# Kernel tuning notes

Hardware: AMD Instinct MI355X
Metric: run time of the kernel (lower is better)

Reference implementation:

```python
import jax, jax.numpy as jnp
import numpy as np

D_MODEL = 1024
NUM_HEADS = 16
HEAD_DIM = D_MODEL // NUM_HEADS


def setup_inputs() -> dict:
    key = jax.random.key(0)
    ks = jax.random.split(key, 9)
    B, S, D = 2, 2048, D_MODEL
    s = 1.0 / np.sqrt(D)
    return {
        "x": jax.random.normal(ks[0], (B, S, D), dtype=jnp.float32),
        "Wq": jax.random.normal(ks[1], (D, D), dtype=jnp.float32) * s,
        "bq": jnp.zeros((D,), dtype=jnp.float32),
        "Wk": jax.random.normal(ks[2], (D, D), dtype=jnp.float32) * s,
        "bk": jnp.zeros((D,), dtype=jnp.float32),
        "Wv": jax.random.normal(ks[3], (D, D), dtype=jnp.float32) * s,
        "bv": jnp.zeros((D,), dtype=jnp.float32),
        "Wo": jax.random.normal(ks[4], (D, D), dtype=jnp.float32) * s,
        "bo": jnp.zeros((D,), dtype=jnp.float32),
    }


def reference(x, Wq, bq, Wk, bk, Wv, bv, Wo, bo):
    B, S, D = x.shape
    H, Hd = NUM_HEADS, HEAD_DIM
    # Linear projections (torch Linear: x @ W^T + b)
    q = (x @ Wq.T + bq).reshape(B, S, H, Hd).transpose(0, 2, 1, 3)  # [B,H,S,Hd]
    k = (x @ Wk.T + bk).reshape(B, S, H, Hd).transpose(0, 2, 1, 3)
    v = (x @ Wv.T + bv).reshape(B, S, H, Hd).transpose(0, 2, 1, 3)
    scale = 1.0 / jnp.sqrt(jnp.asarray(Hd, dtype=x.dtype))
    scores = jnp.einsum("bhqd,bhkd->bhqk", q, k) * scale  # [B,H,S,S]
    causal = jnp.triu(jnp.ones((S, S), dtype=bool), k=1)  # True above diagonal
    scores = jnp.where(causal[None, None], -jnp.inf, scores)
    attn = jax.nn.softmax(scores, axis=-1)
    out = jnp.einsum("bhqk,bhkd->bhqd", attn, v)  # [B,H,S,Hd]
    out = out.transpose(0, 2, 1, 3).reshape(B, S, D)
    return out @ Wo.T + bo
```

## Files before the change

kernel.cpp:

```cpp
#include <hip/hip_runtime.h>

typedef _Float16 f16x8 __attribute__((ext_vector_type(8)));
typedef _Float16 f16x4 __attribute__((ext_vector_type(4)));
typedef float f32x4 __attribute__((ext_vector_type(4)));

#define MFMA32(a, b, c) __builtin_amdgcn_mfma_f32_16x16x32_f16(a, b, c, 0, 0, 0)
#define MFMA16(a, b, c) __builtin_amdgcn_mfma_f32_16x16x16f16(a, b, c, 0, 0, 0)

__global__ __launch_bounds__(256) void convert_all(
    const float* __restrict__ x,
    const float* __restrict__ w0, const float* __restrict__ w1,
    const float* __restrict__ w2, const float* __restrict__ w3,
    _Float16* __restrict__ xb,
    _Float16* __restrict__ o0, _Float16* __restrict__ o1,
    _Float16* __restrict__ o2, _Float16* __restrict__ o3) {
  int chunk = blockIdx.x * 256 + threadIdx.x;
  const float* in;
  _Float16* out;
  int i;
  if (chunk < 1048576) {
    in = x; out = xb; i = chunk * 4;
  } else {
    int t = chunk - 1048576;
    int z = t >> 18;
    i = (t & 262143) * 4;
    in = (z == 0) ? w0 : (z == 1) ? w1 : (z == 2) ? w2 : w3;
    out = (z == 0) ? o0 : (z == 1) ? o1 : (z == 2) ? o2 : o3;
  }
  float4 v = *(const float4*)(in + i);
  f16x4 h;
  h.x = (_Float16)v.x; h.y = (_Float16)v.y; h.z = (_Float16)v.z; h.w = (_Float16)v.w;
  *(f16x4*)(out + i) = h;
}

__device__ __forceinline__ void gld_lds16(_Float16* l, const _Float16* g) {
  __builtin_amdgcn_global_load_lds(
      (const __attribute__((address_space(1))) unsigned int*)g,
      (__attribute__((address_space(3))) unsigned int*)l, 16, 0, 0);
}

__device__ __forceinline__ void stage64(_Float16* lds, const _Float16* g,
                                        int wid, int lane) {
#pragma unroll
  for (int j = 0; j < 2; ++j) {
    int blk = wid * 2 + j;
    int row = blk * 8 + (lane >> 3);
    int col = (lane & 7) * 8;
    gld_lds16(lds + blk * 512, g + (size_t)row * 1024 + col);
  }
}

__device__ __forceinline__ void stage128(_Float16* lds, const _Float16* g,
                                         int wid, int lane) {
#pragma unroll
  for (int j = 0; j < 4; ++j) {
    int blk = wid * 4 + j;
    int row = blk * 8 + (lane >> 3);
    int col = (lane & 7) * 8;
    gld_lds16(lds + blk * 512, g + (size_t)row * 1024 + col);
  }
}

__device__ __forceinline__ void gemm_core64(const _Float16* __restrict__ A,
                                            const _Float16* __restrict__ W,
                                            _Float16* As, _Float16* Bs,
                                            f32x4 acc[4][2], int m0, int n0, int tid) {
  int lane = tid & 63, wid = tid >> 6;
  int lr = lane & 15, lg = lane >> 4;
  int wn = wid * 32;
  for (int k0 = 0; k0 < 1024; k0 += 64) {
    __syncthreads();
    stage64(As, A + (size_t)m0 * 1024 + k0, wid, lane);
    stage128(Bs, W + (size_t)n0 * 1024 + k0, wid, lane);
    __syncthreads();
#pragma unroll
    for (int ks = 0; ks < 2; ++ks) {
      f16x8 af[4], bfv[2];
#pragma unroll
      for (int mf = 0; mf < 4; ++mf)
        af[mf] = *(const f16x8*)(As + (mf * 16 + lr) * 64 + ks * 32 + lg * 8);
#pragma unroll
      for (int nf = 0; nf < 2; ++nf)
        bfv[nf] = *(const f16x8*)(Bs + (wn + nf * 16 + lr) * 64 + ks * 32 + lg * 8);
#pragma unroll
      for (int mf = 0; mf < 4; ++mf)
#pragma unroll
        for (int nf = 0; nf < 2; ++nf)
          acc[mf][nf] = MFMA32(af[mf], bfv[nf], acc[mf][nf]);
    }
  }
}

#define TRP 72

__global__ __launch_bounds__(256) void proj_gemm(
    const _Float16* __restrict__ xb,
    const _Float16* __restrict__ wq, const _Float16* __restrict__ wk,
    const _Float16* __restrict__ wv,
    const float* __restrict__ bq, const float* __restrict__ bk,
    const float* __restrict__ bv,
    _Float16* __restrict__ qo, _Float16* __restrict__ ko, _Float16* __restrict__ vo) {
  __shared__ __align__(16) _Float16 smem[12288];
  _Float16* As = smem;
  _Float16* Bs = smem + 4096;
  int z = blockIdx.z;
  const _Float16* W = (z == 0) ? wq : ((z == 1) ? wk : wv);
  const float* bias = (z == 0) ? bq : ((z == 1) ? bk : bv);
  int tid = threadIdx.x;
  int m0 = blockIdx.x * 64, n0 = blockIdx.y * 128;
  f32x4 acc[4][2] = {};
  gemm_core64(xb, W, As, Bs, acc, m0, n0, tid);

  int lane = tid & 63, wid = tid >> 6;
  int lr = lane & 15, lg = lane >> 4;
  int wn = wid * 32;

  if (z == 2) {
    _Float16* Tr = smem;
    int b = m0 >> 11, s0 = m0 & 2047;
    __syncthreads();
#pragma unroll
    for (int nf = 0; nf < 2; ++nf) {
      int c = wn + nf * 16 + lr;
      float bb = bias[n0 + c];
#pragma unroll
      for (int mf = 0; mf < 4; ++mf)
#pragma unroll
        for (int i = 0; i < 4; ++i)
          Tr[c * TRP + mf * 16 + lg * 4 + i] = (_Float16)(acc[mf][nf][i] + bb);
    }
    __syncthreads();
#pragma unroll
    for (int j = 0; j < 4; ++j) {
      int cid = tid + 256 * j;
      int c = cid >> 3, seg = cid & 7;
      int cg = n0 + c, h = cg >> 6, hd = cg & 63;
      f16x8 v = *(const f16x8*)(Tr + c * TRP + seg * 8);
      *(f16x8*)(vo + ((size_t)(b * 16 + h) * 64 + hd) * 2048 + s0 + seg * 8) = v;
    }
  } else {
    _Float16* o = (z == 0) ? qo : ko;
#pragma unroll
    for (int nf = 0; nf < 2; ++nf) {
      int col = n0 + wn + nf * 16 + lr;
      float bb = bias[col];
      int h = col >> 6, hd = col & 63;
#pragma unroll
      for (int mf = 0; mf < 4; ++mf)
#pragma unroll
        for (int i = 0; i < 4; ++i) {
          int row = m0 + mf * 16 + lg * 4 + i;
          int b = row >> 11, s = row & 2047;
          o[((size_t)(b * 16 + h) * 2048 + s) * 64 + hd] = (_Float16)(acc[mf][nf][i] + bb);
        }
    }
  }
}

__global__ __launch_bounds__(256) void out_gemm(
    const _Float16* __restrict__ attn, const _Float16* __restrict__ wo,
    const float* __restrict__ bo, float* __restrict__ out) {
  __shared__ __align__(16) _Float16 smem[12288];
  _Float16* As = smem;
  _Float16* Bs = smem + 4096;
  int tid = threadIdx.x;
  int m0 = blockIdx.x * 64, n0 = blockIdx.y * 128;
  f32x4 acc[4][2] = {};
  gemm_core64(attn, wo, As, Bs, acc, m0, n0, tid);

  int lane = tid & 63, wid = tid >> 6;
  int lr = lane & 15, lg = lane >> 4;
  int wn = wid * 32;
#pragma unroll
  for (int nf = 0; nf < 2; ++nf) {
    int col = n0 + wn + nf * 16 + lr;
    float bb = bo[col];
#pragma unroll
    for (int mf = 0; mf < 4; ++mf)
#pragma unroll
      for (int i = 0; i < 4; ++i) {
        int row = m0 + mf * 16 + lg * 4 + i;
        out[(size_t)row * 1024 + col] = acc[mf][nf][i] + bb;
      }
  }
}

#define LDP 72

template <bool MASK>
__device__ __forceinline__ void attn_tile32(const _Float16* Ks, const _Float16* Vs,
                                            const f16x8 qb[2][2], int kv0, int qwb,
                                            int lr, int lg,
                                            float m[2], float l[2], f32x4 ot[2][4]) {
  const float L2E = 1.44269504f;
  const float NINF = -__builtin_inff();
  f16x8 kf0[4], kf1[4];
#pragma unroll
  for (int nf = 0; nf < 4; ++nf) {
    kf0[nf] = *(const f16x8*)(Ks + (nf * 16 + lr) * LDP + lg * 8);
    kf1[nf] = *(const f16x8*)(Ks + (nf * 16 + lr) * LDP + 32 + lg * 8);
  }
  f32x4 sc[2][4];
#pragma unroll
  for (int h = 0; h < 2; ++h)
#pragma unroll
    for (int nf = 0; nf < 4; ++nf) {
      f32x4 z = {0.f, 0.f, 0.f, 0.f};
      z = MFMA32(kf0[nf], qb[h][0], z);
      z = MFMA32(kf1[nf], qb[h][1], z);
      sc[h][nf] = z;
    }
  if (MASK) {
#pragma unroll
    for (int h = 0; h < 2; ++h) {
      int qg = qwb + h * 16 + lr;
#pragma unroll
      for (int nf = 0; nf < 4; ++nf)
#pragma unroll
        for (int i = 0; i < 4; ++i) {
          int kg = kv0 + nf * 16 + lg * 4 + i;
          sc[h][nf][i] = (kg <= qg) ? sc[h][nf][i] : NINF;
        }
    }
  }
  f16x4 pf[2][4];
#pragma unroll
  for (int h = 0; h < 2; ++h) {
    f32x4 mx4 = sc[h][0];
#pragma unroll
    for (int nf = 1; nf < 4; ++nf)
#pragma unroll
      for (int i = 0; i < 4; ++i) mx4[i] = fmaxf(mx4[i], sc[h][nf][i]);
    float tm = fmaxf(fmaxf(mx4[0], mx4[1]), fmaxf(mx4[2], mx4[3]));
    tm = fmaxf(tm, __shfl_xor(tm, 16));
    tm = fmaxf(tm, __shfl_xor(tm, 32));
    float mn = fmaxf(m[h], tm);
    float alpha = __builtin_amdgcn_exp2f((m[h] - mn) * L2E);
    m[h] = mn;
    float mnL = mn * L2E;
    float ps = 0.f;
#pragma unroll
    for (int nf = 0; nf < 4; ++nf)
#pragma unroll
      for (int i = 0; i < 4; ++i) {
        float p = __builtin_amdgcn_exp2f(sc[h][nf][i] * L2E - mnL);
        ps += p;
        pf[h][nf][i] = (_Float16)p;
      }
    ps += __shfl_xor(ps, 16);
    ps += __shfl_xor(ps, 32);
    l[h] = l[h] * alpha + ps;
#pragma unroll
    for (int dt = 0; dt < 4; ++dt)
#pragma unroll
      for (int i = 0; i < 4; ++i) ot[h][dt][i] *= alpha;
  }
#pragma unroll
  for (int nf = 0; nf < 4; ++nf)
#pragma unroll
    for (int dt = 0; dt < 4; ++dt) {
      f16x4 vf = *(const f16x4*)(Vs + (dt * 16 + lr) * LDP + nf * 16 + lg * 4);
      ot[0][dt] = MFMA16(vf, pf[0][nf], ot[0][dt]);
      ot[1][dt] = MFMA16(vf, pf[1][nf], ot[1][dt]);
    }
}

__global__ __launch_bounds__(256) void attn_kernel(
    const _Float16* __restrict__ Q, const _Float16* __restrict__ K,
    const _Float16* __restrict__ VT, _Float16* __restrict__ O) {
  __shared__ __align__(16) _Float16 Ks[2][64 * LDP];
  __shared__ __align__(16) _Float16 Vs[2][64 * LDP];
  int tid = threadIdx.x, lane = tid & 63, wid = tid >> 6;
  int hh = blockIdx.x;
  int qt = blockIdx.z ? (15 - (int)blockIdx.y) : (int)blockIdx.y;
  int b = blockIdx.z;
  size_t hoff = (size_t)(b * 16 + hh) * 2048 * 64;
  const _Float16* Qh = Q + hoff;
  const _Float16* Kh = K + hoff;
  const _Float16* VTh = VT + hoff;
  int qwb = qt * 128 + wid * 32;
  int lr = lane & 15, lg = lane >> 4;

  f16x8 qb[2][2];
#pragma unroll
  for (int h = 0; h < 2; ++h) {
    const _Float16* qp = Qh + (size_t)(qwb + h * 16 + lr) * 64;
    qb[h][0] = *(const f16x8*)(qp + lg * 8);
    qb[h][1] = *(const f16x8*)(qp + 32 + lg * 8);
#pragma unroll
    for (int j = 0; j < 8; ++j) {
      qb[h][0][j] *= (_Float16)0.125f;
      qb[h][1][j] *= (_Float16)0.125f;
    }
  }

  float m[2] = {-__builtin_inff(), -__builtin_inff()};
  float l[2] = {0.f, 0.f};
  f32x4 ot[2][4] = {};

  int r0 = tid >> 3, c0 = (tid & 7) * 8;
  int r1 = r0 + 32;
  int4 rk0 = *(const int4*)(Kh + (size_t)r0 * 64 + c0);
  int4 rk1 = *(const int4*)(Kh + (size_t)r1 * 64 + c0);
  int4 rv0 = *(const int4*)(VTh + (size_t)r0 * 2048 + c0);
  int4 rv1 = *(const int4*)(VTh + (size_t)r1 * 2048 + c0);
  *(int4*)(&Ks[0][0] + r0 * LDP + c0) = rk0;
  *(int4*)(&Ks[0][0] + r1 * LDP + c0) = rk1;
  *(int4*)(&Vs[0][0] + r0 * LDP + c0) = rv0;
  *(int4*)(&Vs[0][0] + r1 * LDP + c0) = rv1;
  __syncthreads();

  int aw = qwb >> 6;
  int ntiles = 2 * qt + 2;
  for (int t = 0; t < ntiles; ++t) {
    int cur = t & 1;
    if (t + 1 < ntiles) {
      int nkv = (t + 1) * 64;
      rk0 = *(const int4*)(Kh + (size_t)(nkv + r0) * 64 + c0);
      rk1 = *(const int4*)(Kh + (size_t)(nkv + r1) * 64 + c0);
      rv0 = *(const int4*)(VTh + (size_t)r0 * 2048 + nkv + c0);
      rv1 = *(const int4*)(VTh + (size_t)r1 * 2048 + nkv + c0);
    }
    if (t < aw)
      attn_tile32<false>(&Ks[cur][0], &Vs[cur][0], qb, t * 64, qwb, lr, lg, m, l, ot);
    else if (t == aw)
      attn_tile32<true>(&Ks[cur][0], &Vs[cur][0], qb, t * 64, qwb, lr, lg, m, l, ot);
    if (t + 1 < ntiles) {
      *(int4*)(&Ks[cur ^ 1][0] + r0 * LDP + c0) = rk0;
      *(int4*)(&Ks[cur ^ 1][0] + r1 * LDP + c0) = rk1;
      *(int4*)(&Vs[cur ^ 1][0] + r0 * LDP + c0) = rv0;
      *(int4*)(&Vs[cur ^ 1][0] + r1 * LDP + c0) = rv1;
    }
    __syncthreads();
  }

#pragma unroll
  for (int h = 0; h < 2; ++h) {
    float inv = 1.f / l[h];
    _Float16* Oh = O + ((size_t)b * 2048 + qwb + h * 16 + lr) * 1024 + hh * 64;
#pragma unroll
    for (int dt = 0; dt < 4; ++dt) {
      f16x4 o;
#pragma unroll
      for (int i = 0; i < 4; ++i) o[i] = (_Float16)(ot[h][dt][i] * inv);
      *(f16x4*)(Oh + dt * 16 + lg * 4) = o;
    }
  }
}

extern "C" void kernel_launch(void* const* d_in, const int* in_sizes, int n_in,
                              void* d_out, int out_size, void* d_ws, size_t ws_size,
                              hipStream_t stream) {
  const float* x  = (const float*)d_in[0];
  const float* Wq = (const float*)d_in[1];
  const float* bq = (const float*)d_in[2];
  const float* Wk = (const float*)d_in[3];
  const float* bk = (const float*)d_in[4];
  const float* Wv = (const float*)d_in[5];
  const float* bv = (const float*)d_in[6];
  const float* Wo = (const float*)d_in[7];
  const float* bo = (const float*)d_in[8];
  float* out = (float*)d_out;

  _Float16* ws  = (_Float16*)d_ws;
  _Float16* xb  = ws;
  _Float16* wqb = ws + 4194304;
  _Float16* wkb = ws + 5242880;
  _Float16* wvb = ws + 6291456;
  _Float16* wob = ws + 7340032;
  _Float16* qw  = ws + 8388608;
  _Float16* kw  = ws + 12582912;
  _Float16* vtw = ws + 16777216;
  _Float16* aw  = ws + 20971520;

  convert_all<<<8192, 256, 0, stream>>>(x, Wq, Wk, Wv, Wo,
                                        xb, wqb, wkb, wvb, wob);

  proj_gemm<<<dim3(64, 8, 3), 256, 0, stream>>>(xb, wqb, wkb, wvb, bq, bk, bv,
                                                qw, kw, vtw);
  attn_kernel<<<dim3(16, 16, 2), 256, 0, stream>>>(qw, kw, vtw, aw);
  out_gemm<<<dim3(64, 8), 256, 0, stream>>>(aw, wob, bo, out);
}
```

Baseline: 123.0 us.

## Fuse Q and K projections into one block sharing the staged x tile

The projection kernel now runs Q and K in the same block. The x tile is staged once into shared memory and feeds two accumulator sets, while V keeps its own path. This removes the duplicate x loads for Q and K and cuts the grid from three z-slices to two. In exchange, shared memory per block grows from 24KB to 40KB and accumulator registers double, which may lower occupancy, and the grid shrinks to 1024 blocks with uneven work per block.

```diff
diff --git a/kernel.cpp b/kernel.cpp
--- a/kernel.cpp
+++ b/kernel.cpp
@@ -100,29 +100,72 @@
     const float* __restrict__ bq, const float* __restrict__ bk,
     const float* __restrict__ bv,
     _Float16* __restrict__ qo, _Float16* __restrict__ ko, _Float16* __restrict__ vo) {
-  __shared__ __align__(16) _Float16 smem[12288];
-  _Float16* As = smem;
-  _Float16* Bs = smem + 4096;
-  int z = blockIdx.z;
-  const _Float16* W = (z == 0) ? wq : ((z == 1) ? wk : wv);
-  const float* bias = (z == 0) ? bq : ((z == 1) ? bk : bv);
+  __shared__ __align__(16) _Float16 smem[20480];
   int tid = threadIdx.x;
-  int m0 = blockIdx.x * 64, n0 = blockIdx.y * 128;
-  f32x4 acc[4][2] = {};
-  gemm_core64(xb, W, As, Bs, acc, m0, n0, tid);
-
   int lane = tid & 63, wid = tid >> 6;
   int lr = lane & 15, lg = lane >> 4;
   int wn = wid * 32;
-
-  if (z == 2) {
+  int m0 = blockIdx.x * 64, n0 = blockIdx.y * 128;
+
+  if (blockIdx.z == 0) {
+    _Float16* As = smem;
+    _Float16* Bq = smem + 4096;
+    _Float16* Bk = smem + 12288;
+    f32x4 aq[4][2] = {}, ak[4][2] = {};
+    for (int k0 = 0; k0 < 1024; k0 += 64) {
+      __syncthreads();
+      stage64(As, xb + (size_t)m0 * 1024 + k0, wid, lane);
+      stage128(Bq, wq + (size_t)n0 * 1024 + k0, wid, lane);
+      stage128(Bk, wk + (size_t)n0 * 1024 + k0, wid, lane);
+      __syncthreads();
+#pragma unroll
+      for (int ks = 0; ks < 2; ++ks) {
+        f16x8 af[4], bqf[2], bkf[2];
+#pragma unroll
+        for (int mf = 0; mf < 4; ++mf)
+          af[mf] = *(const f16x8*)(As + (mf * 16 + lr) * 64 + ks * 32 + lg * 8);
+#pragma unroll
+        for (int nf = 0; nf < 2; ++nf) {
+          bqf[nf] = *(const f16x8*)(Bq + (wn + nf * 16 + lr) * 64 + ks * 32 + lg * 8);
+          bkf[nf] = *(const f16x8*)(Bk + (wn + nf * 16 + lr) * 64 + ks * 32 + lg * 8);
+        }
+#pragma unroll
+        for (int mf = 0; mf < 4; ++mf)
+#pragma unroll
+          for (int nf = 0; nf < 2; ++nf) {
+            aq[mf][nf] = MFMA32(af[mf], bqf[nf], aq[mf][nf]);
+            ak[mf][nf] = MFMA32(af[mf], bkf[nf], ak[mf][nf]);
+          }
+      }
+    }
+#pragma unroll
+    for (int nf = 0; nf < 2; ++nf) {
+      int col = n0 + wn + nf * 16 + lr;
+      float bbq = bq[col], bbk = bk[col];
+      int h = col >> 6, hd = col & 63;
+#pragma unroll
+      for (int mf = 0; mf < 4; ++mf)
+#pragma unroll
+        for (int i = 0; i < 4; ++i) {
+          int row = m0 + mf * 16 + lg * 4 + i;
+          int b = row >> 11, s = row & 2047;
+          size_t off = ((size_t)(b * 16 + h) * 2048 + s) * 64 + hd;
+          qo[off] = (_Float16)(aq[mf][nf][i] + bbq);
+          ko[off] = (_Float16)(ak[mf][nf][i] + bbk);
+        }
+    }
+  } else {
+    _Float16* As = smem;
+    _Float16* Bs = smem + 4096;
+    f32x4 acc[4][2] = {};
+    gemm_core64(xb, wv, As, Bs, acc, m0, n0, tid);
     _Float16* Tr = smem;
     int b = m0 >> 11, s0 = m0 & 2047;
     __syncthreads();
 #pragma unroll
     for (int nf = 0; nf < 2; ++nf) {
       int c = wn + nf * 16 + lr;
-      float bb = bias[n0 + c];
+      float bb = bv[n0 + c];
 #pragma unroll
       for (int mf = 0; mf < 4; ++mf)
 #pragma unroll
@@ -137,22 +180,6 @@
       int cg = n0 + c, h = cg >> 6, hd = cg & 63;
       f16x8 v = *(const f16x8*)(Tr + c * TRP + seg * 8);
       *(f16x8*)(vo + ((size_t)(b * 16 + h) * 64 + hd) * 2048 + s0 + seg * 8) = v;
-    }
-  } else {
-    _Float16* o = (z == 0) ? qo : ko;
-#pragma unroll
-    for (int nf = 0; nf < 2; ++nf) {
-      int col = n0 + wn + nf * 16 + lr;
-      float bb = bias[col];
-      int h = col >> 6, hd = col & 63;
-#pragma unroll
-      for (int mf = 0; mf < 4; ++mf)
-#pragma unroll
-        for (int i = 0; i < 4; ++i) {
-          int row = m0 + mf * 16 + lg * 4 + i;
-          int b = row >> 11, s = row & 2047;
-          o[((size_t)(b * 16 + h) * 2048 + s) * 64 + hd] = (_Float16)(acc[mf][nf][i] + bb);
-        }
     }
   }
 }
@@ -376,7 +403,7 @@
   convert_all<<<8192, 256, 0, stream>>>(x, Wq, Wk, Wv, Wo,
                                         xb, wqb, wkb, wvb, wob);
 
-  proj_gemm<<<dim3(64, 8, 3), 256, 0, stream>>>(xb, wqb, wkb, wvb, bq, bk, bv,
+  proj_gemm<<<dim3(64, 8, 2), 256, 0, stream>>>(xb, wqb, wkb, wvb, bq, bk, bv,
                                                 qw, kw, vtw);
   attn_kernel<<<dim3(16, 16, 2), 256, 0, stream>>>(qw, kw, vtw, aw);
   out_gemm<<<dim3(64, 8), 256, 0, stream>>>(aw, wob, bo, out);
```

New measurement: 126.1 us. +2.6%, slower.

## Split KV tiles across two wave groups per attention block and merge softmax

Applied to the files above, without the earlier changes.

The attention block grows to 512 threads in two groups of four waves. Each group processes alternate 64-key tiles of the same 128 queries, staged in four shared-memory buffers loaded per 128-key step. At the end, group B writes its running max, sum and partial outputs to shared memory, and group A merges them with rescaling before writing the output. This doubles the waves in flight to improve latency hiding and MFMA throughput. It costs an extra combine pass through shared memory and more load imbalance on the causal diagonal.

```diff
diff --git a/kernel.cpp b/kernel.cpp
--- a/kernel.cpp
+++ b/kernel.cpp
@@ -265,12 +265,19 @@
     }
 }
 
-__global__ __launch_bounds__(256) void attn_kernel(
+__global__ __launch_bounds__(512, 4) void attn_kernel(
     const _Float16* __restrict__ Q, const _Float16* __restrict__ K,
     const _Float16* __restrict__ VT, _Float16* __restrict__ O) {
-  __shared__ __align__(16) _Float16 Ks[2][64 * LDP];
-  __shared__ __align__(16) _Float16 Vs[2][64 * LDP];
+  __shared__ __align__(16) _Float16 smem[18432];
+  _Float16* KsA = smem;
+  _Float16* KsB = smem + 4608;
+  _Float16* VsA = smem + 9216;
+  _Float16* VsB = smem + 13824;
+  const float L2E = 1.44269504f;
+
   int tid = threadIdx.x, lane = tid & 63, wid = tid >> 6;
+  int grp = wid >> 2;
+  int wq4 = wid & 3;
   int hh = blockIdx.x;
   int qt = blockIdx.z ? (15 - (int)blockIdx.y) : (int)blockIdx.y;
   int b = blockIdx.z;
@@ -278,7 +285,7 @@
   const _Float16* Qh = Q + hoff;
   const _Float16* Kh = K + hoff;
   const _Float16* VTh = VT + hoff;
-  int qwb = qt * 128 + wid * 32;
+  int qwb = qt * 128 + wq4 * 32;
   int lr = lane & 15, lg = lane >> 4;
 
   f16x8 qb[2][2];
@@ -298,52 +305,79 @@
   float l[2] = {0.f, 0.f};
   f32x4 ot[2][4] = {};
 
-  int r0 = tid >> 3, c0 = (tid & 7) * 8;
-  int r1 = r0 + 32;
-  int4 rk0 = *(const int4*)(Kh + (size_t)r0 * 64 + c0);
-  int4 rk1 = *(const int4*)(Kh + (size_t)r1 * 64 + c0);
-  int4 rv0 = *(const int4*)(VTh + (size_t)r0 * 2048 + c0);
-  int4 rv1 = *(const int4*)(VTh + (size_t)r1 * 2048 + c0);
-  *(int4*)(&Ks[0][0] + r0 * LDP + c0) = rk0;
-  *(int4*)(&Ks[0][0] + r1 * LDP + c0) = rk1;
-  *(int4*)(&Vs[0][0] + r0 * LDP + c0) = rv0;
-  *(int4*)(&Vs[0][0] + r1 * LDP + c0) = rv1;
+  int rr = tid >> 3, cc = (tid & 7) * 8;
+  int4 rka = *(const int4*)(Kh + (size_t)rr * 64 + cc);
+  int4 rkb = *(const int4*)(Kh + (size_t)(64 + rr) * 64 + cc);
+  int4 rva = *(const int4*)(VTh + (size_t)rr * 2048 + cc);
+  int4 rvb = *(const int4*)(VTh + (size_t)rr * 2048 + 64 + cc);
+  *(int4*)(KsA + rr * LDP + cc) = rka;
+  *(int4*)(KsB + rr * LDP + cc) = rkb;
+  *(int4*)(VsA + rr * LDP + cc) = rva;
+  *(int4*)(VsB + rr * LDP + cc) = rvb;
   __syncthreads();
 
   int aw = qwb >> 6;
-  int ntiles = 2 * qt + 2;
-  for (int t = 0; t < ntiles; ++t) {
-    int cur = t & 1;
-    if (t + 1 < ntiles) {
-      int nkv = (t + 1) * 64;
-      rk0 = *(const int4*)(Kh + (size_t)(nkv + r0) * 64 + c0);
-      rk1 = *(const int4*)(Kh + (size_t)(nkv + r1) * 64 + c0);
-      rv0 = *(const int4*)(VTh + (size_t)r0 * 2048 + nkv + c0);
-      rv1 = *(const int4*)(VTh + (size_t)r1 * 2048 + nkv + c0);
-    }
-    if (t < aw)
-      attn_tile32<false>(&Ks[cur][0], &Vs[cur][0], qb, t * 64, qwb, lr, lg, m, l, ot);
-    else if (t == aw)
-      attn_tile32<true>(&Ks[cur][0], &Vs[cur][0], qb, t * 64, qwb, lr, lg, m, l, ot);
-    if (t + 1 < ntiles) {
-      *(int4*)(&Ks[cur ^ 1][0] + r0 * LDP + c0) = rk0;
-      *(int4*)(&Ks[cur ^ 1][0] + r1 * LDP + c0) = rk1;
-      *(int4*)(&Vs[cur ^ 1][0] + r0 * LDP + c0) = rv0;
-      *(int4*)(&Vs[cur ^ 1][0] + r1 * LDP + c0) = rv1;
-    }
+  for (int p = 0; p <= qt; ++p) {
+    if (p < qt) {
+      int ka = (p + 1) * 128, kb = ka + 64;
+      rka = *(const int4*)(Kh + (size_t)(ka + rr) * 64 + cc);
+      rkb = *(const int4*)(Kh + (size_t)(kb + rr) * 64 + cc);
+      rva = *(const int4*)(VTh + (size_t)rr * 2048 + ka + cc);
+      rvb = *(const int4*)(VTh + (size_t)rr * 2048 + kb + cc);
+    }
+    int tm = 2 * p + grp;
+    const _Float16* Ks = grp ? KsB : KsA;
+    const _Float16* Vs = grp ? VsB : VsA;
+    if (tm < aw)
+      attn_tile32<false>(Ks, Vs, qb, tm * 64, qwb, lr, lg, m, l, ot);
+    else if (tm == aw)
+      attn_tile32<true>(Ks, Vs, qb, tm * 64, qwb, lr, lg, m, l, ot);
     __syncthreads();
-  }
-
-#pragma unroll
-  for (int h = 0; h < 2; ++h) {
-    float inv = 1.f / l[h];
-    _Float16* Oh = O + ((size_t)b * 2048 + qwb + h * 16 + lr) * 1024 + hh * 64;
-#pragma unroll
-    for (int dt = 0; dt < 4; ++dt) {
-      f16x4 o;
-#pragma unroll
-      for (int i = 0; i < 4; ++i) o[i] = (_Float16)(ot[h][dt][i] * inv);
-      *(f16x4*)(Oh + dt * 16 + lg * 4) = o;
+    if (p < qt) {
+      *(int4*)(KsA + rr * LDP + cc) = rka;
+      *(int4*)(KsB + rr * LDP + cc) = rkb;
+      *(int4*)(VsA + rr * LDP + cc) = rva;
+      *(int4*)(VsB + rr * LDP + cc) = rvb;
+      __syncthreads();
+    }
+  }
+
+  float* Cmb = (float*)smem;
+  if (grp == 1) {
+    int base = wq4 * 64 + lane;
+#pragma unroll
+    for (int h = 0; h < 2; ++h) {
+      Cmb[(h * 18 + 0) * 256 + base] = m[h];
+      Cmb[(h * 18 + 1) * 256 + base] = l[h];
+#pragma unroll
+      for (int dt = 0; dt < 4; ++dt)
+#pragma unroll
+        for (int i = 0; i < 4; ++i)
+          Cmb[(h * 18 + 2 + dt * 4 + i) * 256 + base] = ot[h][dt][i];
+    }
+  }
+  __syncthreads();
+  if (grp == 0) {
+    int base = wq4 * 64 + lane;
+#pragma unroll
+    for (int h = 0; h < 2; ++h) {
+      float mB = Cmb[(h * 18 + 0) * 256 + base];
+      float lB = Cmb[(h * 18 + 1) * 256 + base];
+      float ms = fmaxf(m[h], mB);
+      float fA = __builtin_amdgcn_exp2f((m[h] - ms) * L2E);
+      float fB = __builtin_amdgcn_exp2f((mB - ms) * L2E);
+      float inv = 1.f / (fA * l[h] + fB * lB);
+      fA *= inv; fB *= inv;
+      _Float16* Oh = O + ((size_t)b * 2048 + qwb + h * 16 + lr) * 1024 + hh * 64;
+#pragma unroll
+      for (int dt = 0; dt < 4; ++dt) {
+        f16x4 o;
+#pragma unroll
+        for (int i = 0; i < 4; ++i)
+          o[i] = (_Float16)(fA * ot[h][dt][i] +
+                            fB * Cmb[(h * 18 + 2 + dt * 4 + i) * 256 + base]);
+        *(f16x4*)(Oh + dt * 16 + lg * 4) = o;
+      }
     }
   }
 }
@@ -378,6 +412,6 @@
 
   proj_gemm<<<dim3(64, 8, 3), 256, 0, stream>>>(xb, wqb, wkb, wvb, bq, bk, bv,
                                                 qw, kw, vtw);
-  attn_kernel<<<dim3(16, 16, 2), 256, 0, stream>>>(qw, kw, vtw, aw);
+  attn_kernel<<<dim3(16, 16, 2), 512, 0, stream>>>(qw, kw, vtw, aw);
   out_gemm<<<dim3(64, 8), 256, 0, stream>>>(aw, wob, bo, out);
 }
```

Measured after the change: 131.5 us. 1.07x slower.
